# Kernel optimization log

Hardware: AMD Instinct MI355X
Metric: run time of the kernel (lower is better)

The kernel has to match this reference:

```python
import jax, jax.numpy as jnp
import numpy as np

T, B, V, S = 800, 32, 1024, 100
BLANK = 0
LS = 0.1
NEG = -1e10  # finite 'log-zero' to keep grads NaN-free


def setup_inputs() -> dict:
    key = jax.random.key(0)
    k1, k2, k3, k4 = jax.random.split(key, 4)
    logits = jax.random.normal(k1, (T, B, V), jnp.float32)
    log_probs = jax.nn.log_softmax(logits, axis=-1)  # (T,B,V) as F.ctc_loss expects
    targets = jax.random.randint(k2, (B, S), 1, V)   # non-blank labels
    input_lengths = jax.random.randint(k3, (B,), T // 2, T + 1)
    target_lengths = jax.random.randint(k4, (B,), S // 2, S + 1)
    return dict(log_probs=log_probs, targets=targets,
                input_lengths=input_lengths, target_lengths=target_lengths)


def _ctc_loss_mean(log_probs, targets, input_lengths, target_lengths):
    # log_probs: (T,B,V); targets: (B,S)
    Tt, Bb, Vv = log_probs.shape
    Ss = targets.shape[1]
    L = 2 * Ss + 1  # extended label sequence: blank-interleaved
    ext = jnp.full((Bb, L), BLANK, dtype=targets.dtype).at[:, 1::2].set(targets)
    ext_prev2 = jnp.pad(ext[:, :-2], ((0, 0), (2, 0)), constant_values=BLANK)
    # transition s-2 -> s allowed only for non-blank labels differing from two back
    can_skip = (ext != BLANK) & (ext != ext_prev2)  # (B,L)

    def emit(lp_t):  # (B,V) -> (B,L) emission log-probs of extended labels
        return jnp.take_along_axis(lp_t, ext, axis=1)

    e0 = emit(log_probs[0])
    alpha0 = jnp.full((Bb, L), NEG, dtype=log_probs.dtype)
    alpha0 = alpha0.at[:, 0].set(e0[:, 0]).at[:, 1].set(e0[:, 1])

    def step(alpha, xs):
        lp_t, t = xs
        a1 = jnp.pad(alpha[:, :-1], ((0, 0), (1, 0)), constant_values=NEG)
        a2 = jnp.pad(alpha[:, :-2], ((0, 0), (2, 0)), constant_values=NEG)
        new = jnp.logaddexp(alpha, a1)
        new = jnp.where(can_skip, jnp.logaddexp(new, a2), new) + emit(lp_t)
        # freeze alpha for t >= input_length so final carry == alpha at len-1
        alpha = jnp.where((t < input_lengths)[:, None], new, alpha)
        return alpha, None

    alpha_T, _ = jax.lax.scan(step, alpha0, (log_probs[1:], jnp.arange(1, Tt)))

    idx = 2 * target_lengths  # final blank position in extended sequence
    a_blank = jnp.take_along_axis(alpha_T, idx[:, None], axis=1)[:, 0]
    a_label = jnp.take_along_axis(alpha_T, (idx - 1)[:, None], axis=1)[:, 0]
    nll = -jnp.logaddexp(a_blank, a_label)  # (B,)
    nll = jnp.where(nll > 1e9, 0.0, nll)    # zero_infinity
    # reduction='mean': per-sample loss / target_length, then batch mean
    return jnp.mean(nll / target_lengths.astype(log_probs.dtype))


def reference(log_probs, targets, input_lengths, target_lengths):
    ctc = _ctc_loss_mean(log_probs, targets, input_lengths, target_lengths)
    smooth = -jnp.mean(log_probs)
    return (1.0 - LS) * ctc + LS * smooth
```

## Files before the change

kernel.cpp:

```cpp
#include <hip/hip_runtime.h>
#include <hip/hip_bf16.h>

#define T_DIM 800
#define B_DIM 32
#define V_DIM 1024
#define S_DIM 100
#define L2E  1.4426950408889634f
#define LN2  0.6931471805599453f

#define NB1  1600
#define EOFF 4096
#define EROW 128
#define BROWS 801


__device__ __forceinline__ float dpp_shr1_f(float x) {
    return __int_as_float(__builtin_amdgcn_update_dpp(
        0, __float_as_int(x), 0x138, 0xF, 0xF, false));
}
__device__ __forceinline__ int dpp_shr1_i(int x) {
    return __builtin_amdgcn_update_dpp(0, x, 0x138, 0xF, 0xF, false);
}
__device__ __forceinline__ float rl50(float x) {
    return __int_as_float(__builtin_amdgcn_readlane(__float_as_int(x), 50));
}
__device__ __forceinline__ void gl16(const float* g, float* lds_dst) {
    __builtin_amdgcn_global_load_lds(
        (const __attribute__((address_space(1))) unsigned int*)g,
        (__attribute__((address_space(3))) unsigned int*)lds_dst,
        16, 0, 0);
}

extern "C" __global__ void __launch_bounds__(256)
ctc_prep(const float* __restrict__ lp,
         const int* __restrict__ tgt,
         float* __restrict__ ws)
{
    __shared__ float rb[4][2][V_DIM];
    __shared__ float red[4];
    float* E = ws + EOFF;
    float* partials = ws + 1;
    const int bid = blockIdx.x;
    const int tid = threadIdx.x;
    const int w = tid >> 6, j = tid & 63;
    const int b  = bid / 50;
    const int t0 = (bid - b * 50) * 16 + w * 4;
    const int* tg = tgt + b * S_DIM;

    if (bid == 0 && tid == 0) ((unsigned int*)ws)[0] = 0;

    int c1 = 0, c2 = 0;
    if (j <= 49) { int2 t2 = ((const int2*)tg)[j]; c1 = t2.x; c2 = t2.y; }

    float s = 0.0f;
    #pragma unroll
    for (int i = 0; i < 4; ++i) {
        const int t = t0 + i;
        const float4* src = (const float4*)(lp + ((size_t)t * B_DIM + b) * V_DIM);
        float4 va = src[j], vb = src[j + 64], vc = src[j + 128], vd = src[j + 192];
        s += ((va.x + va.y) + (va.z + va.w)) + ((vb.x + vb.y) + (vb.z + vb.w))
           + ((vc.x + vc.y) + (vc.z + vc.w)) + ((vd.x + vd.y) + (vd.z + vd.w));
        float* rw = rb[w][i & 1];
        ((float4*)rw)[j] = va; ((float4*)rw)[j + 64] = vb;
        ((float4*)rw)[j + 128] = vc; ((float4*)rw)[j + 192] = vd;
        float a, c;
        if (j <= 49)      { a = __builtin_amdgcn_exp2f(rw[c1] * L2E);
                            c = __builtin_amdgcn_exp2f(rw[c2] * L2E); }
        else if (j == 50) { float ebv = __builtin_amdgcn_exp2f(rw[0] * L2E);
                            a = ebv; c = ebv; }
        else              { a = 0.0f; c = 0.0f; }
        ((float2*)(E + ((size_t)b * BROWS + t) * EROW))[j] = make_float2(a, c);
    }
    for (int off = 32; off; off >>= 1) s += __shfl_down(s, off, 64);
    if (j == 0) red[w] = s;
    __syncthreads();
    if (tid == 0) partials[bid] = (red[0] + red[1]) + (red[2] + red[3]);
}

extern "C" __global__ void __launch_bounds__(128)
ctc_rec(const int* __restrict__ tgt,
        const int* __restrict__ ilen,
        const int* __restrict__ tlen,
        float* __restrict__ ws,
        float* __restrict__ out)
{
    __shared__ float bufA[32 * EROW];
    __shared__ float bufB[32 * EROW];
    unsigned int* cnt = (unsigned int*)ws;
    float* partials = ws + 1;
    float* nlls = ws + 1 + NB1;
    const int b = blockIdx.x;
    const int tid = threadIdx.x;
    const int wav = tid >> 6;
    const int l = tid & 63;
    const float* E = ws + EOFF + (size_t)b * BROWS * EROW;
    const int* tg = tgt + b * S_DIM;
    const int len = ilen[b];
    const int tl  = tlen[b];
    const int steps = len - 1;
    const int nfull = steps >> 5;
    const int nst   = steps & 31;
    const int N     = nfull + (nst ? 1 : 0);

#define STAGE_P(BUFP, SB) do { \
    const int tb_ = 1 + 32 * (SB); \
    float* bp_ = (BUFP); \
    _Pragma("unroll") \
    for (int g_ = 0; g_ < 16; ++g_) { \
        gl16(E + (size_t)(tb_ + 2 * g_) * EROW + 4 * l, bp_ + g_ * 256); \
    } \
} while (0)

#define WAIT0 do { \
    asm volatile("s_waitcnt vmcnt(0)" ::: "memory"); \
    __builtin_amdgcn_sched_barrier(0); \
} while (0)

    if (wav == 1) {
        STAGE_P(bufA, 0); WAIT0;
        __builtin_amdgcn_s_barrier();
        #pragma unroll 1
        for (int k = 1; k < N; ++k) {
            STAGE_P((k & 1) ? bufB : bufA, k); WAIT0;
            __builtin_amdgcn_s_barrier();
        }
        return;
    }

    float cs1f = 0, cs3f = 0;
    if (l <= 49) {
        int v1 = tg[2 * l];
        int vp = (l >= 1) ? tg[2 * l - 1] : -1;
        cs1f = (v1 != vp) ? 1.0f : 0.0f;
        int v3 = tg[2 * l + 1];
        cs3f = (v3 != v1) ? 1.0f : 0.0f;
    }

    float p0 = 0, p1 = 0, p2 = 0, p3 = 0;
    float qv = 0, sff = 0, sfg = 0;
    int   el = 0, eLp = 0;
    {
        float2 q0 = ((const float2*)E)[l];
        float eb0 = rl50(q0.x);
        p0 = (l == 0) ? eb0  : 0.0f;
        p1 = (l == 0) ? q0.x : 0.0f;
    }

    float2 ga0, ga1, ga2, ga3, gb0, gb1, gb2, gb3;

#define PREF_(BUF, G, R0, R1, R2, R3) do { \
    const float2* bp_ = (const float2*)(BUF); \
    R0 = bp_[(4 * (G) + 0) * 64 + l]; \
    R1 = bp_[(4 * (G) + 1) * 64 + l]; \
    R2 = bp_[(4 * (G) + 2) * 64 + l]; \
    R3 = bp_[(4 * (G) + 3) * 64 + l]; \
} while (0)

#define BD do { \
    float mz_ = fmaxf(fmaxf(p0, p1), fmaxf(p2, p3)); \
    int dead_ = (mz_ == 0.0f) ? 1 : 0; \
    int er_ = (int)((__float_as_uint(mz_) >> 23) & 255u); \
    unsigned fld_ = dead_ ? 127u : (unsigned)(254 - er_); \
    float sc_ = __uint_as_float(fld_ << 23); \
    p0 *= sc_; p1 *= sc_; p2 *= sc_; p3 *= sc_; \
    el += dead_ ? 0 : (er_ - 127); \
    int e1s_ = dpp_shr1_i(el); \
    int elA_ = dead_ ? e1s_ : el; \
    int e2s_ = dpp_shr1_i(elA_); \
    int elB_ = dead_ ? e2s_ : el; \
    int e3s_ = dpp_shr1_i(elB_); \
    int d1_ = e3s_ - elB_; d1_ = d1_ < -120 ? -120 : (d1_ > 120 ? 120 : d1_); \
    int d2_ = eLp  - elB_; d2_ = d2_ < -120 ? -120 : (d2_ > 120 ? 120 : d2_); \
    sfg = (l == 0) ? 0.0f : __uint_as_float((unsigned)(d1_ + 127) << 23); \
    sff = (l == 0) ? 0.0f : __uint_as_float((unsigned)(d2_ + 127) << 23); \
    el = elB_; eLp = e3s_; \
} while (0)

#define ST(SF, Q, EBS) do { \
    float h3_ = qv * (SF); \
    float vown_ = fmaf(cs3f, p1, p2 + p3); \
    float n3_ = vown_ * (Q).y; \
    float n0_ = (p0 + h3_) * (EBS); \
    float n1_ = fmaf(cs1f, h3_, p0 + p1) * (Q).x; \
    float n2_ = (p1 + p2) * (EBS); \
    qv = dpp_shr1_f(n3_); \
    p0 = n0_; p1 = n1_; p2 = n2_; p3 = n3_; \
} while (0)

#define GRP_(R0, R1, R2, R3) do { \
    BD; \
    ST(sff, R0, rl50(R0.x)); \
    ST(sfg, R1, rl50(R1.x)); \
    ST(sfg, R2, rl50(R2.x)); \
    ST(sfg, R3, rl50(R3.x)); \
} while (0)

#define GRPT_(R0, R1, R2, R3, BASE) do { \
    if ((BASE) < nst) { \
        BD; \
        ST(sff, R0, rl50(R0.x)); \
        if ((BASE) + 1 < nst) ST(sfg, R1, rl50(R1.x)); \
        if ((BASE) + 2 < nst) ST(sfg, R2, rl50(R2.x)); \
        if ((BASE) + 3 < nst) ST(sfg, R3, rl50(R3.x)); \
    } \
} while (0)

#define CONS_FULL(BUF) do { \
    PREF_(BUF, 0, ga0, ga1, ga2, ga3); \
    PREF_(BUF, 1, gb0, gb1, gb2, gb3); GRP_(ga0, ga1, ga2, ga3); \
    PREF_(BUF, 2, ga0, ga1, ga2, ga3); GRP_(gb0, gb1, gb2, gb3); \
    PREF_(BUF, 3, gb0, gb1, gb2, gb3); GRP_(ga0, ga1, ga2, ga3); \
    PREF_(BUF, 4, ga0, ga1, ga2, ga3); GRP_(gb0, gb1, gb2, gb3); \
    PREF_(BUF, 5, gb0, gb1, gb2, gb3); GRP_(ga0, ga1, ga2, ga3); \
    PREF_(BUF, 6, ga0, ga1, ga2, ga3); GRP_(gb0, gb1, gb2, gb3); \
    PREF_(BUF, 7, gb0, gb1, gb2, gb3); GRP_(ga0, ga1, ga2, ga3); \
    GRP_(gb0, gb1, gb2, gb3); \
} while (0)

#define CONS_TAIL(BUF) do { \
    PREF_(BUF, 0, ga0, ga1, ga2, ga3); \
    PREF_(BUF, 1, gb0, gb1, gb2, gb3); GRPT_(ga0, ga1, ga2, ga3, 0); \
    PREF_(BUF, 2, ga0, ga1, ga2, ga3); GRPT_(gb0, gb1, gb2, gb3, 4); \
    PREF_(BUF, 3, gb0, gb1, gb2, gb3); GRPT_(ga0, ga1, ga2, ga3, 8); \
    PREF_(BUF, 4, ga0, ga1, ga2, ga3); GRPT_(gb0, gb1, gb2, gb3, 12); \
    PREF_(BUF, 5, gb0, gb1, gb2, gb3); GRPT_(ga0, ga1, ga2, ga3, 16); \
    PREF_(BUF, 6, ga0, ga1, ga2, ga3); GRPT_(gb0, gb1, gb2, gb3, 20); \
    PREF_(BUF, 7, gb0, gb1, gb2, gb3); GRPT_(ga0, ga1, ga2, ga3, 24); \
    GRPT_(gb0, gb1, gb2, gb3, 28); \
} while (0)

    __builtin_amdgcn_s_barrier();
    #pragma unroll 1
    for (int k = 0; k + 1 < N; ++k) {
        const float* cur = (k & 1) ? bufB : bufA;
        CONS_FULL(cur);
        __builtin_amdgcn_s_barrier();
    }
    {
        const float* cur = ((N - 1) & 1) ? bufB : bufA;
        if (nst) { CONS_TAIL(cur); } else { CONS_FULL(cur); }
    }

    int idx = 2 * tl;
    int lanehi = idx >> 2, rhi = idx & 3;
    int lanelo = (idx - 1) >> 2, rlo = (idx - 1) & 3;
    float q0 = __shfl(p0, lanehi, 64), q1 = __shfl(p1, lanehi, 64);
    float q2 = __shfl(p2, lanehi, 64), q3 = __shfl(p3, lanehi, 64);
    int   eh = __shfl(el, lanehi, 64);
    float ph = (rhi == 0) ? q0 : (rhi == 1) ? q1 : (rhi == 2) ? q2 : q3;
    float g0 = __shfl(p0, lanelo, 64), g1 = __shfl(p1, lanelo, 64);
    float g2 = __shfl(p2, lanelo, 64), g3 = __shfl(p3, lanelo, 64);
    int   eo = __shfl(el, lanelo, 64);
    float pl = (rlo == 0) ? g0 : (rlo == 1) ? g1 : (rlo == 2) ? g2 : g3;
    float vhi = (ph > 0.0f) ? __builtin_amdgcn_logf(ph) + (float)eh : -3.0e9f;
    float vlo = (pl > 0.0f) ? __builtin_amdgcn_logf(pl) + (float)eo : -3.0e9f;
    float m = fmaxf(vhi, vlo);
    float d = fminf(vhi, vlo) - m;
    float ll2 = m + __builtin_amdgcn_logf(1.0f + __builtin_amdgcn_exp2f(d));
    float nll = -ll2 * LN2;
    if (!(nll < 1e9f)) nll = 0.0f;

    int last = 0;
    if (l == 0) {
        nlls[b] = nll;
        __threadfence();
        unsigned old = __hip_atomic_fetch_add(cnt, 1u, __ATOMIC_ACQ_REL,
                                              __HIP_MEMORY_SCOPE_AGENT);
        last = (old == B_DIM - 1) ? 1 : 0;
    }
    last = __shfl(last, 0, 64);
    if (last) {
        float ps = 0.0f;
        for (int i = l; i < NB1; i += 64) ps += partials[i];
        for (int off = 32; off; off >>= 1) ps += __shfl_down(ps, off, 64);
        float cs = 0.0f;
        if (l < B_DIM) cs = nlls[l] / (float)tlen[l];
        for (int off = 32; off; off >>= 1) cs += __shfl_down(cs, off, 64);
        if (l == 0) {
            float smooth = -ps / (float)((long long)T_DIM * B_DIM * V_DIM);
            float ctc = cs / (float)B_DIM;
            out[0] = 0.9f * ctc + 0.1f * smooth;
        }
    }
}

extern "C" void kernel_launch(void* const* d_in, const int* in_sizes, int n_in,
                              void* d_out, int out_size, void* d_ws, size_t ws_size,
                              hipStream_t stream) {
    const float* lp  = (const float*)d_in[0];
    const int* tgt   = (const int*)d_in[1];
    const int* ilen  = (const int*)d_in[2];
    const int* tlen  = (const int*)d_in[3];
    float* out = (float*)d_out;
    float* ws  = (float*)d_ws;
    ctc_prep<<<NB1, 256, 0, stream>>>(lp, tgt, ws);
    ctc_rec<<<B_DIM, 128, 0, stream>>>(tgt, ilen, tlen, ws, out);
}
```

Before: 64.59 us.

## Fuse prep and recursion kernels with per-chunk ready flags

Merges the emission-prep kernel and the CTC recursion kernel into a single launch. The first 32 blocks run the recursion and spin on per-(batch, time-chunk) flags written by the prep blocks, so the recursion can start while prep is still running and the kernel boundary goes away. A memset clears the counter and flags, and three loader waves split the staging. This relies on all blocks being co-resident or scheduled in order (a deadlock risk), and it adds a memset launch plus spin-polling traffic.

```diff
diff --git a/kernel.cpp b/kernel.cpp
--- a/kernel.cpp
+++ b/kernel.cpp
@@ -8,7 +8,7 @@
 #define L2E  1.4426950408889634f
 #define LN2  0.6931471805599453f
 
-#define NB1  1600
+#define NPREP 1600
 #define EOFF 4096
 #define EROW 128
 #define BROWS 801
@@ -32,69 +32,74 @@
 }
 
 extern "C" __global__ void __launch_bounds__(256)
-ctc_prep(const float* __restrict__ lp,
-         const int* __restrict__ tgt,
-         float* __restrict__ ws)
+ctc_fused(const float* __restrict__ lp,
+          const int* __restrict__ tgt,
+          const int* __restrict__ ilen,
+          const int* __restrict__ tlen,
+          float* __restrict__ ws,
+          float* __restrict__ out)
 {
-    __shared__ float rb[4][2][V_DIM];
+    __shared__ float smem[8192];
     __shared__ float red[4];
-    float* E = ws + EOFF;
-    float* partials = ws + 1;
+    unsigned int* cnt = (unsigned int*)ws;
+    unsigned int* flagv = (unsigned int*)ws + 1;
+    float* partials = ws + 1601;
+    float* nlls = ws + 3201;
+    float* Eall = ws + EOFF;
     const int bid = blockIdx.x;
     const int tid = threadIdx.x;
     const int w = tid >> 6, j = tid & 63;
-    const int b  = bid / 50;
-    const int t0 = (bid - b * 50) * 16 + w * 4;
+
+    if (bid >= B_DIM) {
+        const int bp = bid - B_DIM;
+        const int b  = bp & 31;
+        const int chunk = bp >> 5;
+        const int t0 = chunk * 16 + w * 4;
+        const int* tg = tgt + b * S_DIM;
+        float* E = Eall + (size_t)b * BROWS * EROW;
+        float* rb = smem + w * 2048;
+
+        int c1 = 0, c2 = 0;
+        if (j <= 49) { int2 t2 = ((const int2*)tg)[j]; c1 = t2.x; c2 = t2.y; }
+
+        float s = 0.0f;
+        #pragma unroll
+        for (int i = 0; i < 4; ++i) {
+            const int t = t0 + i;
+            const float4* src = (const float4*)(lp + ((size_t)t * B_DIM + b) * V_DIM);
+            float4 va = src[j], vb = src[j + 64], vc = src[j + 128], vd = src[j + 192];
+            s += ((va.x + va.y) + (va.z + va.w)) + ((vb.x + vb.y) + (vb.z + vb.w))
+               + ((vc.x + vc.y) + (vc.z + vc.w)) + ((vd.x + vd.y) + (vd.z + vd.w));
+            float* rw = rb + (i & 1) * 1024;
+            ((float4*)rw)[j] = va; ((float4*)rw)[j + 64] = vb;
+            ((float4*)rw)[j + 128] = vc; ((float4*)rw)[j + 192] = vd;
+            float a, c;
+            if (j <= 49)      { a = __builtin_amdgcn_exp2f(rw[c1] * L2E);
+                                c = __builtin_amdgcn_exp2f(rw[c2] * L2E); }
+            else if (j == 50) { float ebv = __builtin_amdgcn_exp2f(rw[0] * L2E);
+                                a = ebv; c = ebv; }
+            else              { a = 0.0f; c = 0.0f; }
+            ((float2*)(E + (size_t)t * EROW))[j] = make_float2(a, c);
+        }
+        for (int off = 32; off; off >>= 1) s += __shfl_down(s, off, 64);
+        if (j == 0) red[w] = s;
+        __syncthreads();
+        if (tid == 0) {
+            partials[bp] = (red[0] + red[1]) + (red[2] + red[3]);
+            __threadfence();
+            __hip_atomic_store(&flagv[b * 50 + chunk], 1u,
+                               __ATOMIC_RELAXED, __HIP_MEMORY_SCOPE_AGENT);
+        }
+        return;
+    }
+
+    float* bufA = smem;
+    float* bufB = smem + 4096;
+    const int b = bid;
+    const int l = j;
+    const float* E = Eall + (size_t)b * BROWS * EROW;
     const int* tg = tgt + b * S_DIM;
-
-    if (bid == 0 && tid == 0) ((unsigned int*)ws)[0] = 0;
-
-    int c1 = 0, c2 = 0;
-    if (j <= 49) { int2 t2 = ((const int2*)tg)[j]; c1 = t2.x; c2 = t2.y; }
-
-    float s = 0.0f;
-    #pragma unroll
-    for (int i = 0; i < 4; ++i) {
-        const int t = t0 + i;
-        const float4* src = (const float4*)(lp + ((size_t)t * B_DIM + b) * V_DIM);
-        float4 va = src[j], vb = src[j + 64], vc = src[j + 128], vd = src[j + 192];
-        s += ((va.x + va.y) + (va.z + va.w)) + ((vb.x + vb.y) + (vb.z + vb.w))
-           + ((vc.x + vc.y) + (vc.z + vc.w)) + ((vd.x + vd.y) + (vd.z + vd.w));
-        float* rw = rb[w][i & 1];
-        ((float4*)rw)[j] = va; ((float4*)rw)[j + 64] = vb;
-        ((float4*)rw)[j + 128] = vc; ((float4*)rw)[j + 192] = vd;
-        float a, c;
-        if (j <= 49)      { a = __builtin_amdgcn_exp2f(rw[c1] * L2E);
-                            c = __builtin_amdgcn_exp2f(rw[c2] * L2E); }
-        else if (j == 50) { float ebv = __builtin_amdgcn_exp2f(rw[0] * L2E);
-                            a = ebv; c = ebv; }
-        else              { a = 0.0f; c = 0.0f; }
-        ((float2*)(E + ((size_t)b * BROWS + t) * EROW))[j] = make_float2(a, c);
-    }
-    for (int off = 32; off; off >>= 1) s += __shfl_down(s, off, 64);
-    if (j == 0) red[w] = s;
-    __syncthreads();
-    if (tid == 0) partials[bid] = (red[0] + red[1]) + (red[2] + red[3]);
-}
-
-extern "C" __global__ void __launch_bounds__(128)
-ctc_rec(const int* __restrict__ tgt,
-        const int* __restrict__ ilen,
-        const int* __restrict__ tlen,
-        float* __restrict__ ws,
-        float* __restrict__ out)
-{
-    __shared__ float bufA[32 * EROW];
-    __shared__ float bufB[32 * EROW];
-    unsigned int* cnt = (unsigned int*)ws;
-    float* partials = ws + 1;
-    float* nlls = ws + 1 + NB1;
-    const int b = blockIdx.x;
-    const int tid = threadIdx.x;
-    const int wav = tid >> 6;
-    const int l = tid & 63;
-    const float* E = ws + EOFF + (size_t)b * BROWS * EROW;
-    const int* tg = tgt + b * S_DIM;
+    const unsigned int* flb = flagv + b * 50;
     const int len = ilen[b];
     const int tl  = tlen[b];
     const int steps = len - 1;
@@ -102,26 +107,26 @@
     const int nst   = steps & 31;
     const int N     = nfull + (nst ? 1 : 0);
 
-#define STAGE_P(BUFP, SB) do { \
-    const int tb_ = 1 + 32 * (SB); \
-    float* bp_ = (BUFP); \
-    _Pragma("unroll") \
-    for (int g_ = 0; g_ < 16; ++g_) { \
-        gl16(E + (size_t)(tb_ + 2 * g_) * EROW + 4 * l, bp_ + g_ * 256); \
-    } \
-} while (0)
-
+#define SPIN1(c) while (__hip_atomic_load(flb + (c), __ATOMIC_RELAXED, \
+                        __HIP_MEMORY_SCOPE_AGENT) == 0) {}
 #define WAIT0 do { \
     asm volatile("s_waitcnt vmcnt(0)" ::: "memory"); \
     __builtin_amdgcn_sched_barrier(0); \
 } while (0)
 
-    if (wav == 1) {
-        STAGE_P(bufA, 0); WAIT0;
-        __builtin_amdgcn_s_barrier();
+    if (w != 0) {
         #pragma unroll 1
-        for (int k = 1; k < N; ++k) {
-            STAGE_P((k & 1) ? bufB : bufA, k); WAIT0;
+        for (int k = 0; k < N; ++k) {
+            int clo = 2 * k, cmid = 2 * k + 1, chi = 2 * k + 2;
+            if (chi > 49) chi = 49;
+            SPIN1(clo); SPIN1(cmid); SPIN1(chi);
+            __threadfence();
+            const int tb_ = 1 + 32 * k;
+            float* bp_ = (k & 1) ? bufB : bufA;
+            for (int g = w - 1; g < 16; g += 3) {
+                gl16(E + (size_t)(tb_ + 2 * g) * EROW + 4 * l, bp_ + g * 256);
+            }
+            WAIT0;
             __builtin_amdgcn_s_barrier();
         }
         return;
@@ -140,6 +145,8 @@
     float qv = 0, sff = 0, sfg = 0;
     int   el = 0, eLp = 0;
     {
+        SPIN1(0);
+        __threadfence();
         float2 q0 = ((const float2*)E)[l];
         float eb0 = rl50(q0.x);
         p0 = (l == 0) ? eb0  : 0.0f;
@@ -271,7 +278,7 @@
     last = __shfl(last, 0, 64);
     if (last) {
         float ps = 0.0f;
-        for (int i = l; i < NB1; i += 64) ps += partials[i];
+        for (int i = l; i < NPREP; i += 64) ps += partials[i];
         for (int off = 32; off; off >>= 1) ps += __shfl_down(ps, off, 64);
         float cs = 0.0f;
         if (l < B_DIM) cs = nlls[l] / (float)tlen[l];
@@ -293,6 +300,6 @@
     const int* tlen  = (const int*)d_in[3];
     float* out = (float*)d_out;
     float* ws  = (float*)d_ws;
-    ctc_prep<<<NB1, 256, 0, stream>>>(lp, tgt, ws);
-    ctc_rec<<<B_DIM, 128, 0, stream>>>(tgt, ilen, tlen, ws, out);
-}
+    hipMemsetAsync(d_ws, 0, 4 * (1 + 1600), stream);
+    ctc_fused<<<B_DIM + NPREP, 256, 0, stream>>>(lp, tgt, ilen, tlen, ws, out);
+}
```

Measured after the change: 139.3 us. 2.16x slower.
